# Performance work log

Measured on AMD Instinct MI355X. Metric: run time of the kernel, lower is better.

The kernel has to match this reference:

```python
import jax, jax.numpy as jnp
import numpy as np

ALPHA = 0.5  # LeakyReLU negative slope


def setup_inputs() -> dict:
    key = jax.random.key(0)
    k1, k2, k3, k4, k5 = jax.random.split(key, 5)
    B, N, S, SO, K = 16, 2048, 12, 12, 32
    return {
        "fushed_features": jax.random.normal(k1, (B, N, 64), dtype=jnp.float32),
        "input_data": jax.random.normal(k2, (B, N, S), dtype=jnp.float32),
        "W": jax.random.normal(k3, (S, SO), dtype=jnp.float32) * (1.414 / np.sqrt(S)),
        "a": jax.random.normal(k4, (2 * SO, 1), dtype=jnp.float32) * 0.3,
        "idx": jax.random.randint(k5, (B, N, K), 0, N, dtype=jnp.int32),
    }


def reference(fushed_features, input_data, W, a, idx):
    # input_data: (B, N, S); W: (S, SO); a: (2*SO, 1); idx: (B, N, K)
    B, N, S = input_data.shape
    SO = W.shape[1]
    wh = input_data @ W  # (B, N, SO)
    # concat([wh_i, wh_j]) @ a  ==  wh_i @ a[:SO] + wh_j @ a[SO:]  (exact same math,
    # avoids materializing the (B,N,N,2*SO) concat the torch code builds)
    e_src = wh @ a[:SO, 0]  # (B, N)
    e_dst = wh @ a[SO:, 0]  # (B, N)
    scores = jax.nn.leaky_relu(e_src[:, :, None] + e_dst[:, None, :], negative_slope=ALPHA)  # (B,N,N)
    att = jnp.take_along_axis(scores, idx, axis=2)  # (B, N, K) gather top-k neighbor scores
    att = jax.nn.softmax(att, axis=-1)  # softmax over the K neighbors
    # gather neighbor time series: (B, N, K, S)
    neigh = input_data[jnp.arange(B)[:, None, None], idx]
    out = att[..., None] * neigh  # (B, N, K, S)
    return out
```

## Files before the change

kernel.cpp:

```cpp
#include <hip/hip_runtime.h>


#define GAT_N 2048
#define GAT_ALPHA 0.5f
#define PPBLK 128
#define THREADS 1024

__global__ __launch_bounds__(THREADS, 1) void gat_lds(
    const float* __restrict__ x,
    const float* __restrict__ W,
    const float* __restrict__ a,
    const int*   __restrict__ idx,
    float*       __restrict__ out)
{
    __shared__ float rows[GAT_N * 12];
    __shared__ float edt[GAT_N];
    __shared__ float es_loc[PPBLK];

    const int tid   = threadIdx.x;
    const int b     = blockIdx.x >> 4;
    const int blk16 = blockIdx.x & 15;

    const int slot   = tid >> 5;
    const int k      = tid & 31;
    const int pairG0 = (b << 11) + blk16 * PPBLK + slot;

    int jv[4];
    #pragma unroll
    for (int t = 0; t < 4; ++t)
        jv[t] = idx[(size_t)(pairG0 + 32 * t) * 32 + k];

    const float4* gp = (const float4*)(x + (size_t)b * GAT_N * 12 + (size_t)tid * 24);
    const float4 v0 = gp[0], v1 = gp[1], v2 = gp[2];
    const float4 v3 = gp[3], v4 = gp[4], v5 = gp[5];

    float acc;
    {
        const int l     = tid & 63;
        const int idx24 = l % 24;
        const int s     = idx24 % 12;
        const float* av = a + (idx24 < 12 ? 0 : 12);
        acc = 0.f;
        #pragma unroll
        for (int t = 0; t < 12; ++t) acc += W[s * 12 + t] * av[t];
    }
    float wvd[12];
    #pragma unroll
    for (int s = 0; s < 12; ++s) wvd[s] = __shfl(acc, 12 + s, 64);

    const float ed0 =
        v0.x*wvd[0] + v0.y*wvd[1] + v0.z*wvd[2]  + v0.w*wvd[3] +
        v1.x*wvd[4] + v1.y*wvd[5] + v1.z*wvd[6]  + v1.w*wvd[7] +
        v2.x*wvd[8] + v2.y*wvd[9] + v2.z*wvd[10] + v2.w*wvd[11];
    const float ed1 =
        v3.x*wvd[0] + v3.y*wvd[1] + v3.z*wvd[2]  + v3.w*wvd[3] +
        v4.x*wvd[4] + v4.y*wvd[5] + v4.z*wvd[6]  + v4.w*wvd[7] +
        v5.x*wvd[8] + v5.y*wvd[9] + v5.z*wvd[10] + v5.w*wvd[11];

    if ((tid >> 6) == blk16) {
        float wvs[12];
        #pragma unroll
        for (int s = 0; s < 12; ++s) wvs[s] = __shfl(acc, s, 64);
        const float es0 =
            v0.x*wvs[0] + v0.y*wvs[1] + v0.z*wvs[2]  + v0.w*wvs[3] +
            v1.x*wvs[4] + v1.y*wvs[5] + v1.z*wvs[6]  + v1.w*wvs[7] +
            v2.x*wvs[8] + v2.y*wvs[9] + v2.z*wvs[10] + v2.w*wvs[11];
        const float es1 =
            v3.x*wvs[0] + v3.y*wvs[1] + v3.z*wvs[2]  + v3.w*wvs[3] +
            v4.x*wvs[4] + v4.y*wvs[5] + v4.z*wvs[6]  + v4.w*wvs[7] +
            v5.x*wvs[8] + v5.y*wvs[9] + v5.z*wvs[10] + v5.w*wvs[11];
        const int local2 = 2 * tid - blk16 * PPBLK;
        es_loc[local2]     = es0;
        es_loc[local2 + 1] = es1;
    }

    {
        float4* lp = (float4*)(rows + tid * 24);
        lp[0] = v0; lp[1] = v1; lp[2] = v2;
        lp[3] = v3; lp[4] = v4; lp[5] = v5;
        *(float2*)(edt + 2 * tid) = make_float2(ed0, ed1);
    }
    __syncthreads();

    float ex[4], sum[4];
    #pragma unroll
    for (int t = 0; t < 4; ++t) {
        float e = es_loc[slot + 32 * t] + edt[jv[t]];
        e = e > 0.f ? e : GAT_ALPHA * e;
        ex[t]  = __expf(fminf(e, 80.f));
        sum[t] = ex[t];
    }
    #pragma unroll
    for (int off = 16; off; off >>= 1) {
        #pragma unroll
        for (int t = 0; t < 4; ++t) sum[t] += __shfl_xor(sum[t], off, 32);
    }
    float att[4];
    #pragma unroll
    for (int t = 0; t < 4; ++t) att[t] = ex[t] / sum[t];

    #pragma unroll
    for (int t = 0; t < 4; ++t) {
        float4* o4 = (float4*)out + (size_t)(pairG0 + 32 * t) * 96;
        #pragma unroll
        for (int r = 0; r < 3; ++r) {
            const int f  = r * 32 + k;
            const int kk = f / 3;
            const int q  = f - 3 * kk;
            const float attk = __shfl(att[t], kk, 32);
            const int   jk   = __shfl(jv[t],  kk, 32);
            const float4 v = *(const float4*)(rows + jk * 12 + 4 * q);
            o4[f] = make_float4(attk * v.x, attk * v.y, attk * v.z, attk * v.w);
        }
    }
}

__global__ __launch_bounds__(256) void gat_fused(
    const float* __restrict__ x, const float* __restrict__ W,
    const float* __restrict__ a, const int* __restrict__ idx,
    float* __restrict__ out)
{
    __shared__ float wvec[24];
    __shared__ float stage[8 * 384];
    const int tid = threadIdx.x;

    if (tid < 24) {
        const int s = tid % 12;
        const float* av = a + (tid < 12 ? 0 : 12);
        float acc = 0.f;
        #pragma unroll
        for (int t = 0; t < 12; ++t) acc += W[s * 12 + t] * av[t];
        wvec[tid] = acc;
    }
    __syncthreads();

    const int p    = tid >> 5;
    const int pair = blockIdx.x * 8 + p;
    const int k    = tid & 31;

    const float4* rowi = (const float4*)(x + (size_t)pair * 12);
    const float4 i0 = rowi[0], i1 = rowi[1], i2 = rowi[2];
    const float e_src =
        i0.x*wvec[0] + i0.y*wvec[1] + i0.z*wvec[2]  + i0.w*wvec[3] +
        i1.x*wvec[4] + i1.y*wvec[5] + i1.z*wvec[6]  + i1.w*wvec[7] +
        i2.x*wvec[8] + i2.y*wvec[9] + i2.z*wvec[10] + i2.w*wvec[11];

    const int j   = idx[(size_t)pair * 32 + k];
    const int nbr = (pair & ~(GAT_N - 1)) + j;
    const float4* rowj = (const float4*)(x + (size_t)nbr * 12);
    const float4 n0 = rowj[0], n1 = rowj[1], n2 = rowj[2];
    const float e_dst =
        n0.x*wvec[12] + n0.y*wvec[13] + n0.z*wvec[14] + n0.w*wvec[15] +
        n1.x*wvec[16] + n1.y*wvec[17] + n1.z*wvec[18] + n1.w*wvec[19] +
        n2.x*wvec[20] + n2.y*wvec[21] + n2.z*wvec[22] + n2.w*wvec[23];

    float sc = e_src + e_dst;
    sc = sc > 0.f ? sc : GAT_ALPHA * sc;
    float m = sc;
    #pragma unroll
    for (int off = 16; off; off >>= 1) m = fmaxf(m, __shfl_xor(m, off, 32));
    const float ex = __expf(sc - m);
    float sum = ex;
    #pragma unroll
    for (int off = 16; off; off >>= 1) sum += __shfl_xor(sum, off, 32);
    const float att = ex / sum;

    float4* st = (float4*)(stage + p * 384 + k * 12);
    st[0] = make_float4(att * n0.x, att * n0.y, att * n0.z, att * n0.w);
    st[1] = make_float4(att * n1.x, att * n1.y, att * n1.z, att * n1.w);
    st[2] = make_float4(att * n2.x, att * n2.y, att * n2.z, att * n2.w);
    __syncthreads();

    const float4* sm4 = (const float4*)stage;
    float4* o4 = (float4*)(out + (size_t)blockIdx.x * 8 * 384);
    #pragma unroll
    for (int r = 0; r < 3; ++r) o4[tid + 256 * r] = sm4[tid + 256 * r];
}

extern "C" void kernel_launch(void* const* d_in, const int* in_sizes, int n_in,
                              void* d_out, int out_size, void* d_ws, size_t ws_size,
                              hipStream_t stream) {
    const float* x   = (const float*)d_in[1];
    const float* W   = (const float*)d_in[2];
    const float* a   = (const float*)d_in[3];
    const int*   idx = (const int*)d_in[4];
    float* out = (float*)d_out;

    const int pairs = in_sizes[1] / 12;

    if ((pairs & (GAT_N - 1)) == 0) {
        gat_lds<<<pairs / PPBLK, THREADS, 0, stream>>>(x, W, a, idx, out);
    } else {
        gat_fused<<<pairs / 8, 256, 0, stream>>>(x, W, a, idx, out);
    }
}
```

Before: 85.56 us.

## Halve block size to 512 threads and swizzle blocks across XCDs by batch

Each block now handles 64 query nodes with 512 threads instead of 128 nodes with 1024. That doubles the block count, and each thread loads four input rows into LDS instead of two. A block-index swizzle is added when there are exactly 512 blocks, so that the blocks of the same batch land on the same XCD and its L2 sees reuse of that batch's x rows and idx. The cost is that every block re-stages the full 96KB batch slab into LDS, and the number of such redundant loads doubles.

```diff
diff --git a/kernel.cpp b/kernel.cpp
--- a/kernel.cpp
+++ b/kernel.cpp
@@ -3,89 +3,102 @@
 
 #define GAT_N 2048
 #define GAT_ALPHA 0.5f
-#define PPBLK 128
-#define THREADS 1024
-
-__global__ __launch_bounds__(THREADS, 1) void gat_lds(
+#define PPBLK 64
+#define THREADS 512
+
+__global__ __launch_bounds__(THREADS) void gat_lds2(
     const float* __restrict__ x,
     const float* __restrict__ W,
     const float* __restrict__ a,
     const int*   __restrict__ idx,
-    float*       __restrict__ out)
+    float*       __restrict__ out,
+    const int    swz)
 {
     __shared__ float rows[GAT_N * 12];
     __shared__ float edt[GAT_N];
     __shared__ float es_loc[PPBLK];
 
-    const int tid   = threadIdx.x;
-    const int b     = blockIdx.x >> 4;
-    const int blk16 = blockIdx.x & 15;
+    const int tid = threadIdx.x;
+    int b, blk32;
+    if (swz) {
+        const int xcd = blockIdx.x & 7;
+        const int i   = blockIdx.x >> 3;
+        b     = (xcd << 1) | (i >> 5);
+        blk32 = i & 31;
+    } else {
+        b     = blockIdx.x >> 5;
+        blk32 = blockIdx.x & 31;
+    }
 
     const int slot   = tid >> 5;
     const int k      = tid & 31;
-    const int pairG0 = (b << 11) + blk16 * PPBLK + slot;
+    const int pairG0 = b * GAT_N + blk32 * PPBLK + slot;
 
     int jv[4];
     #pragma unroll
     for (int t = 0; t < 4; ++t)
-        jv[t] = idx[(size_t)(pairG0 + 32 * t) * 32 + k];
-
-    const float4* gp = (const float4*)(x + (size_t)b * GAT_N * 12 + (size_t)tid * 24);
-    const float4 v0 = gp[0], v1 = gp[1], v2 = gp[2];
-    const float4 v3 = gp[3], v4 = gp[4], v5 = gp[5];
+        jv[t] = idx[(size_t)(pairG0 + 16 * t) * 32 + k];
 
     float acc;
     {
         const int l     = tid & 63;
-        const int idx24 = l % 24;
-        const int s     = idx24 % 12;
-        const float* av = a + (idx24 < 12 ? 0 : 12);
+        const int id24  = l % 24;
+        const int s     = id24 % 12;
+        const float* av = a + (id24 < 12 ? 0 : 12);
         acc = 0.f;
         #pragma unroll
         for (int t = 0; t < 12; ++t) acc += W[s * 12 + t] * av[t];
     }
-    float wvd[12];
-    #pragma unroll
-    for (int s = 0; s < 12; ++s) wvd[s] = __shfl(acc, 12 + s, 64);
-
-    const float ed0 =
-        v0.x*wvd[0] + v0.y*wvd[1] + v0.z*wvd[2]  + v0.w*wvd[3] +
-        v1.x*wvd[4] + v1.y*wvd[5] + v1.z*wvd[6]  + v1.w*wvd[7] +
-        v2.x*wvd[8] + v2.y*wvd[9] + v2.z*wvd[10] + v2.w*wvd[11];
-    const float ed1 =
-        v3.x*wvd[0] + v3.y*wvd[1] + v3.z*wvd[2]  + v3.w*wvd[3] +
-        v4.x*wvd[4] + v4.y*wvd[5] + v4.z*wvd[6]  + v4.w*wvd[7] +
-        v5.x*wvd[8] + v5.y*wvd[9] + v5.z*wvd[10] + v5.w*wvd[11];
-
-    if ((tid >> 6) == blk16) {
-        float wvs[12];
-        #pragma unroll
-        for (int s = 0; s < 12; ++s) wvs[s] = __shfl(acc, s, 64);
-        const float es0 =
-            v0.x*wvs[0] + v0.y*wvs[1] + v0.z*wvs[2]  + v0.w*wvs[3] +
-            v1.x*wvs[4] + v1.y*wvs[5] + v1.z*wvs[6]  + v1.w*wvs[7] +
-            v2.x*wvs[8] + v2.y*wvs[9] + v2.z*wvs[10] + v2.w*wvs[11];
-        const float es1 =
-            v3.x*wvs[0] + v3.y*wvs[1] + v3.z*wvs[2]  + v3.w*wvs[3] +
-            v4.x*wvs[4] + v4.y*wvs[5] + v4.z*wvs[6]  + v4.w*wvs[7] +
-            v5.x*wvs[8] + v5.y*wvs[9] + v5.z*wvs[10] + v5.w*wvs[11];
-        const int local2 = 2 * tid - blk16 * PPBLK;
-        es_loc[local2]     = es0;
-        es_loc[local2 + 1] = es1;
-    }
-
-    {
-        float4* lp = (float4*)(rows + tid * 24);
+    float ws[12], wd[12];
+    #pragma unroll
+    for (int s = 0; s < 12; ++s) {
+        ws[s] = __shfl(acc, s, 64);
+        wd[s] = __shfl(acc, 12 + s, 64);
+    }
+
+    const bool own_es = (tid >> 4) == blk32;
+    #pragma unroll
+    for (int c = 0; c < 2; ++c) {
+        const float4* gp = (const float4*)(x + (size_t)b * GAT_N * 12
+                                             + (size_t)tid * 48 + c * 24);
+        const float4 v0 = gp[0], v1 = gp[1], v2 = gp[2];
+        const float4 v3 = gp[3], v4 = gp[4], v5 = gp[5];
+
+        const float ed0 =
+            v0.x*wd[0] + v0.y*wd[1] + v0.z*wd[2]  + v0.w*wd[3] +
+            v1.x*wd[4] + v1.y*wd[5] + v1.z*wd[6]  + v1.w*wd[7] +
+            v2.x*wd[8] + v2.y*wd[9] + v2.z*wd[10] + v2.w*wd[11];
+        const float ed1 =
+            v3.x*wd[0] + v3.y*wd[1] + v3.z*wd[2]  + v3.w*wd[3] +
+            v4.x*wd[4] + v4.y*wd[5] + v4.z*wd[6]  + v4.w*wd[7] +
+            v5.x*wd[8] + v5.y*wd[9] + v5.z*wd[10] + v5.w*wd[11];
+
+        const int nb = 4 * tid + 2 * c;
+        float4* lp = (float4*)(rows + (size_t)nb * 12);
         lp[0] = v0; lp[1] = v1; lp[2] = v2;
         lp[3] = v3; lp[4] = v4; lp[5] = v5;
-        *(float2*)(edt + 2 * tid) = make_float2(ed0, ed1);
+        *(float2*)(edt + nb) = make_float2(ed0, ed1);
+
+        if (own_es) {
+            const float es0 =
+                v0.x*ws[0] + v0.y*ws[1] + v0.z*ws[2]  + v0.w*ws[3] +
+                v1.x*ws[4] + v1.y*ws[5] + v1.z*ws[6]  + v1.w*ws[7] +
+                v2.x*ws[8] + v2.y*ws[9] + v2.z*ws[10] + v2.w*ws[11];
+            const float es1 =
+                v3.x*ws[0] + v3.y*ws[1] + v3.z*ws[2]  + v3.w*ws[3] +
+                v4.x*ws[4] + v4.y*ws[5] + v4.z*ws[6]  + v4.w*ws[7] +
+                v5.x*ws[8] + v5.y*ws[9] + v5.z*ws[10] + v5.w*ws[11];
+            const int loc = (tid & 15) * 4 + 2 * c;
+            es_loc[loc]     = es0;
+            es_loc[loc + 1] = es1;
+        }
     }
     __syncthreads();
 
     float ex[4], sum[4];
     #pragma unroll
     for (int t = 0; t < 4; ++t) {
-        float e = es_loc[slot + 32 * t] + edt[jv[t]];
+        float e = es_loc[slot + 16 * t] + edt[jv[t]];
         e = e > 0.f ? e : GAT_ALPHA * e;
         ex[t]  = __expf(fminf(e, 80.f));
         sum[t] = ex[t];
@@ -101,7 +114,7 @@
 
     #pragma unroll
     for (int t = 0; t < 4; ++t) {
-        float4* o4 = (float4*)out + (size_t)(pairG0 + 32 * t) * 96;
+        float4* o4 = (float4*)out + (size_t)(pairG0 + 16 * t) * 96;
         #pragma unroll
         for (int r = 0; r < 3; ++r) {
             const int f  = r * 32 + k;
@@ -109,7 +122,7 @@
             const int q  = f - 3 * kk;
             const float attk = __shfl(att[t], kk, 32);
             const int   jk   = __shfl(jv[t],  kk, 32);
-            const float4 v = *(const float4*)(rows + jk * 12 + 4 * q);
+            const float4 v = *(const float4*)(rows + (size_t)jk * 12 + 4 * q);
             o4[f] = make_float4(attk * v.x, attk * v.y, attk * v.z, attk * v.w);
         }
     }
@@ -189,7 +202,9 @@
     const int pairs = in_sizes[1] / 12;
 
     if ((pairs & (GAT_N - 1)) == 0) {
-        gat_lds<<<pairs / PPBLK, THREADS, 0, stream>>>(x, W, a, idx, out);
+        const int blocks = pairs / PPBLK;
+        const int swz    = (blocks == 512) ? 1 : 0;
+        gat_lds2<<<blocks, THREADS, 0, stream>>>(x, W, a, idx, out, swz);
     } else {
         gat_fused<<<pairs / 8, 256, 0, stream>>>(x, W, a, idx, out);
     }
```

Result: slower. 87.73 us (+2.5%).
